# Kernel optimization log

Measured on AMD Instinct MI355X. Metric: run time of the kernel, lower is better.

The kernel has to match this reference:

```python
import jax, jax.numpy as jnp
import numpy as np


def setup_inputs() -> dict:
    key = jax.random.key(0)
    ip = jax.random.normal(key, (8, 256, 128, 128), dtype=jnp.float32)
    return {"ip": ip}


def reference(ip):
    b, C, H, W = ip.shape
    two_c = 2 * C
    # precomputed complex shift grid: exp(-1j*2*pi*(C-0.5)*v/(2C)), v = 0..2C-1
    v = jnp.arange(two_c, dtype=jnp.float32)
    angle = -2.0 * jnp.pi * (C - 0.5) * v / two_c
    shift = (jnp.cos(angle) + 1j * jnp.sin(angle)).astype(jnp.complex64)  # [2C]

    viDct = ip * two_c                                   # [b, C, H, W]
    flip_neg = -viDct[:, 1:][:, ::-1]                    # [b, C-1, H, W]
    zeros = jnp.zeros((b, 1, H, W), dtype=ip.dtype)
    rev = jnp.concatenate([viDct, zeros, flip_neg], axis=1)  # [b, 2C, H, W]
    rev = rev.astype(jnp.complex64) * shift[None, :, None, None]
    vxx = jnp.fft.ifft(rev, axis=1)                      # norm='backward' (default)
    out = vxx[:, :C][:, ::-1].real                       # first C, flipped, real part
    return out.astype(ip.dtype)
```

## Files before the change

### kernel.cpp

```cpp
#include <hip/hip_runtime.h>
#include <hip/hip_bf16.h>
#include <math.h>

#define NB   8
#define NC   256
#define NHW  (128 * 128)

#define BN 64

typedef __attribute__((ext_vector_type(4))) float f32x4;
typedef __attribute__((ext_vector_type(8))) short bf16x8;

__device__ __forceinline__ unsigned f2bf_lo(float f) {
    unsigned u = __builtin_bit_cast(unsigned, f);
    u += 0x7fffu + ((u >> 16) & 1u);
    return u >> 16;
}
__device__ __forceinline__ unsigned f2bf_hi(float f) {
    unsigned u = __builtin_bit_cast(unsigned, f);
    u += 0x7fffu + ((u >> 16) & 1u);
    return u & 0xffff0000u;
}

__global__ void coef_kernel(unsigned short* __restrict__ coef) {
    int idx = blockIdx.x * 256 + threadIdx.x;
    int c = idx >> 8;
    int k = idx & 255;
    int t = (k * (2 * c + 1)) & 1023;
    float v = (k == 0) ? 1.0f : 2.0f * cosf((float)t * (float)(M_PI / 512.0));
    coef[idx] = (unsigned short)f2bf_lo(v);
}

__device__ __forceinline__ int swz_off(int row, int chunk) {
    return row * 512 + ((chunk ^ (row & 7)) << 4);
}

__global__ __launch_bounds__(512, 4)
void dct_gemm(const float* __restrict__ X, const unsigned short* __restrict__ Mcoef,
              float* __restrict__ Out) {
    __shared__ unsigned char Xlds[BN * 512];

    const int tid  = threadIdx.x;
    const int lane = tid & 63;
    const int wave = tid >> 6;
    const int wm   = wave >> 1;
    const int wn   = wave & 1;
    const int m16  = lane & 15;
    const int quad = lane >> 4;

    const int p0 = blockIdx.x * BN;
    const float* Xb = X + (size_t)blockIdx.y * (NC * NHW);
    float* Ob = Out + (size_t)blockIdx.y * (NC * NHW);

    const int sr = tid & 63;
    const int sh = tid >> 6;
    const float* xsrc = Xb + (size_t)(sh * 32) * NHW + p0 + sr;

#pragma unroll
    for (int half = 0; half < 2; ++half) {
        float v[16];
#pragma unroll
        for (int j = 0; j < 16; j++) v[j] = xsrc[(half * 16 + j) * NHW];
#pragma unroll
        for (int cc = 0; cc < 2; cc++) {
            int chunk = sh * 4 + half * 2 + cc;
            int pk[4];
#pragma unroll
            for (int q = 0; q < 4; q++)
                pk[q] = (int)(f2bf_lo(v[cc * 8 + 2 * q]) | f2bf_hi(v[cc * 8 + 2 * q + 1]));
            *(int4*)(Xlds + swz_off(sr, chunk)) = (int4){pk[0], pk[1], pk[2], pk[3]};
        }
    }
    __syncthreads();

    f32x4 acc[4][2];
#pragma unroll
    for (int i = 0; i < 4; i++)
#pragma unroll
        for (int j = 0; j < 2; j++) acc[i][j] = (f32x4){0.f, 0.f, 0.f, 0.f};

    const unsigned short* Abase = Mcoef + (wm * 64 + m16) * NC + quad * 8;
    const int brow0 = wn * 32 + m16;

#pragma unroll
    for (int s = 0; s < 8; ++s) {
        bf16x8 afr[4], bfr[2];
#pragma unroll
        for (int mt = 0; mt < 4; mt++)
            afr[mt] = *(const bf16x8*)(Abase + mt * 16 * NC + s * 32);
#pragma unroll
        for (int nt = 0; nt < 2; nt++)
            bfr[nt] = *(const bf16x8*)(Xlds + swz_off(brow0 + nt * 16, s * 4 + quad));
#pragma unroll
        for (int mt = 0; mt < 4; mt++)
#pragma unroll
            for (int nt = 0; nt < 2; nt++)
                acc[mt][nt] = __builtin_amdgcn_mfma_f32_16x16x32_bf16(
                    afr[mt], bfr[nt], acc[mt][nt], 0, 0, 0);
    }

#pragma unroll
    for (int mt = 0; mt < 4; mt++) {
#pragma unroll
        for (int nt = 0; nt < 2; nt++) {
            int cc = wm * 64 + mt * 16 + quad * 4;
            int pp = p0 + wn * 32 + nt * 16 + m16;
            float* o = Ob + cc * NHW + pp;
#pragma unroll
            for (int r = 0; r < 4; r++)
                o[r * NHW] = acc[mt][nt][r];
        }
    }
}

extern "C" void kernel_launch(void* const* d_in, const int* in_sizes, int n_in,
                              void* d_out, int out_size, void* d_ws, size_t ws_size,
                              hipStream_t stream) {
    const float* ip = (const float*)d_in[0];
    float* out = (float*)d_out;
    unsigned short* coef = (unsigned short*)d_ws;

    coef_kernel<<<dim3(256), dim3(256), 0, stream>>>(coef);

    dim3 grid(NHW / BN, NB);
    dct_gemm<<<grid, dim3(512), 0, stream>>>(ip, coef, out);
}
```

Baseline: 268.7 us.

## Swap GEMM operand roles for vectorized float4 loads and stores, larger pixel tile

Doubles the pixel tile to 128 and the block to 1024 threads, and swaps the MFMA operand roles so the pixel dimension maps to the accumulator rows. Each thread can then load input as float4 along pixels and store output as float4 rows instead of scalar strided accesses. A new XOR swizzle for the LDS tile is meant to keep bank conflicts low with the transposed write pattern. The risks are lower occupancy from the larger block and LDS footprint, and narrower 8-byte LDS writes.

Result: slower. 276.5 us (+2.9%).

```diff
diff --git a/kernel.cpp b/kernel.cpp
--- a/kernel.cpp
+++ b/kernel.cpp
@@ -5,8 +5,7 @@
 #define NB   8
 #define NC   256
 #define NHW  (128 * 128)
-
-#define BN 64
+#define BN   128
 
 typedef __attribute__((ext_vector_type(4))) float f32x4;
 typedef __attribute__((ext_vector_type(8))) short bf16x8;
@@ -31,84 +30,84 @@
     coef[idx] = (unsigned short)f2bf_lo(v);
 }
 
-__device__ __forceinline__ int swz_off(int row, int chunk) {
-    return row * 512 + ((chunk ^ (row & 7)) << 4);
+__device__ __forceinline__ int xoff(int p, int k8) {
+    return p * 512 + (((k8 ^ (((p >> 2) & 7) << 1))) << 3);
 }
 
-__global__ __launch_bounds__(512, 4)
+__global__ __launch_bounds__(1024, 4)
 void dct_gemm(const float* __restrict__ X, const unsigned short* __restrict__ Mcoef,
               float* __restrict__ Out) {
     __shared__ unsigned char Xlds[BN * 512];
 
-    const int tid  = threadIdx.x;
-    const int lane = tid & 63;
-    const int wave = tid >> 6;
-    const int wm   = wave >> 1;
-    const int wn   = wave & 1;
-    const int m16  = lane & 15;
-    const int quad = lane >> 4;
-
-    const int p0 = blockIdx.x * BN;
+    const int tid = threadIdx.x;
+    const int p0  = blockIdx.x * BN;
     const float* Xb = X + (size_t)blockIdx.y * (NC * NHW);
     float* Ob = Out + (size_t)blockIdx.y * (NC * NHW);
 
-    const int sr = tid & 63;
-    const int sh = tid >> 6;
-    const float* xsrc = Xb + (size_t)(sh * 32) * NHW + p0 + sr;
-
+    {
+        const int pl = tid & 31;
+        const int kq = tid >> 5;
+        const float* xsrc = Xb + p0 + pl * 4;
 #pragma unroll
-    for (int half = 0; half < 2; ++half) {
-        float v[16];
+        for (int o = 0; o < 2; ++o) {
+            const int k0 = o * 128 + kq * 4;
+            f32x4 L[4];
 #pragma unroll
-        for (int j = 0; j < 16; j++) v[j] = xsrc[(half * 16 + j) * NHW];
+            for (int r = 0; r < 4; ++r)
+                L[r] = *(const f32x4*)(xsrc + (size_t)(k0 + r) * NHW);
+            const int k8 = k0 >> 2;
 #pragma unroll
-        for (int cc = 0; cc < 2; cc++) {
-            int chunk = sh * 4 + half * 2 + cc;
-            int pk[4];
-#pragma unroll
-            for (int q = 0; q < 4; q++)
-                pk[q] = (int)(f2bf_lo(v[cc * 8 + 2 * q]) | f2bf_hi(v[cc * 8 + 2 * q + 1]));
-            *(int4*)(Xlds + swz_off(sr, chunk)) = (int4){pk[0], pk[1], pk[2], pk[3]};
+            for (int s = 0; s < 4; ++s) {
+                unsigned w0 = f2bf_lo(L[0][s]) | f2bf_hi(L[1][s]);
+                unsigned w1 = f2bf_lo(L[2][s]) | f2bf_hi(L[3][s]);
+                *(int2*)(Xlds + xoff(pl * 4 + s, k8)) = (int2){(int)w0, (int)w1};
+            }
         }
     }
     __syncthreads();
 
-    f32x4 acc[4][2];
+    const int lane = tid & 63;
+    const int wave = tid >> 6;
+    const int wp   = wave & 3;
+    const int wc   = wave >> 2;
+    const int m16  = lane & 15;
+    const int quad = lane >> 4;
+
+    f32x4 acc[2][4];
 #pragma unroll
-    for (int i = 0; i < 4; i++)
+    for (int i = 0; i < 2; i++)
 #pragma unroll
-        for (int j = 0; j < 2; j++) acc[i][j] = (f32x4){0.f, 0.f, 0.f, 0.f};
+        for (int j = 0; j < 4; j++) acc[i][j] = (f32x4){0.f, 0.f, 0.f, 0.f};
 
-    const unsigned short* Abase = Mcoef + (wm * 64 + m16) * NC + quad * 8;
-    const int brow0 = wn * 32 + m16;
+    const unsigned short* Bbase = Mcoef + (wc * 64 + m16) * NC + quad * 8;
 
 #pragma unroll
     for (int s = 0; s < 8; ++s) {
-        bf16x8 afr[4], bfr[2];
+        bf16x8 afr[2], bfr[4];
 #pragma unroll
-        for (int mt = 0; mt < 4; mt++)
-            afr[mt] = *(const bf16x8*)(Abase + mt * 16 * NC + s * 32);
+        for (int mt = 0; mt < 2; mt++) {
+            int p = wp * 32 + mt * 16 + m16;
+            int pos = (s * 8 + quad * 2) ^ ((((p >> 2) & 7)) << 1);
+            afr[mt] = *(const bf16x8*)(Xlds + p * 512 + (pos << 3));
+        }
 #pragma unroll
-        for (int nt = 0; nt < 2; nt++)
-            bfr[nt] = *(const bf16x8*)(Xlds + swz_off(brow0 + nt * 16, s * 4 + quad));
+        for (int nt = 0; nt < 4; nt++)
+            bfr[nt] = *(const bf16x8*)(Bbase + nt * 16 * NC + s * 32);
 #pragma unroll
-        for (int mt = 0; mt < 4; mt++)
+        for (int mt = 0; mt < 2; mt++)
 #pragma unroll
-            for (int nt = 0; nt < 2; nt++)
+            for (int nt = 0; nt < 4; nt++)
                 acc[mt][nt] = __builtin_amdgcn_mfma_f32_16x16x32_bf16(
                     afr[mt], bfr[nt], acc[mt][nt], 0, 0, 0);
     }
 
 #pragma unroll
-    for (int mt = 0; mt < 4; mt++) {
+    for (int mt = 0; mt < 2; mt++) {
 #pragma unroll
-        for (int nt = 0; nt < 2; nt++) {
-            int cc = wm * 64 + mt * 16 + quad * 4;
-            int pp = p0 + wn * 32 + nt * 16 + m16;
-            float* o = Ob + cc * NHW + pp;
-#pragma unroll
-            for (int r = 0; r < 4; r++)
-                o[r * NHW] = acc[mt][nt][r];
+        for (int nt = 0; nt < 4; nt++) {
+            int cc = wc * 64 + nt * 16 + m16;
+            int pp = p0 + wp * 32 + mt * 16 + quad * 4;
+            *(f32x4*)(Ob + (size_t)cc * NHW + pp) = acc[mt][nt];
         }
     }
 }
@@ -123,5 +122,5 @@
     coef_kernel<<<dim3(256), dim3(256), 0, stream>>>(coef);
 
     dim3 grid(NHW / BN, NB);
-    dct_gemm<<<grid, dim3(512), 0, stream>>>(ip, coef, out);
+    dct_gemm<<<grid, dim3(1024), 0, stream>>>(ip, coef, out);
 }
```
